# Optimization experiments

Measured on AMD Instinct MI355X. Metric: run time of the kernel, lower is better.

## Reference

```python
import jax, jax.numpy as jnp
import numpy as np

N_NODES = 50000
N_EDGES = 800000
IN_CH = 64
HID_CH = 128


def setup_inputs() -> dict:
    key = jax.random.key(0)
    k1, k2, k3 = jax.random.split(key, 3)
    x = jax.random.normal(k1, (N_NODES, IN_CH), dtype=jnp.float32)
    edge_index = jax.random.randint(k2, (2, N_EDGES), 0, N_NODES, dtype=jnp.int64)
    # lin_l weight of SAGEConv: [hidden_channels, in_channels]
    W = jax.random.normal(k3, (HID_CH, IN_CH), dtype=jnp.float32) * (1.0 / np.sqrt(IN_CH))
    return {"x": x, "edge_index": edge_index, "W": W}


def reference(x, edge_index, W):
    src = edge_index[0]  # message sources
    dst = edge_index[1]  # aggregation targets
    msgs = x[src]  # [E, in] gather
    summed = jax.ops.segment_sum(msgs, dst, num_segments=N_NODES)  # [N, in]
    counts = jax.ops.segment_sum(jnp.ones((msgs.shape[0],), dtype=x.dtype), dst,
                                 num_segments=N_NODES)  # [N]
    mean = summed / jnp.maximum(counts, 1.0)[:, None]  # mean aggregation (0 for isolated nodes)
    # lin_l: no bias, no root_weight -> out = mean @ W^T
    return jnp.einsum('ni,oi->no', mean, W)
```

## Files before the change

### kernel.cpp

```cpp
#include <hip/hip_runtime.h>


constexpr int N_NODES = 50000;
constexpr int N_EDGES = 800000;
constexpr int IN_CH   = 64;
constexpr int HID_CH  = 128;

constexpr int NBKT          = 256;
constexpr int NODES_PER_BKT = 196;
constexpr int BKT_CAP       = 4096;
constexpr int CHUNK         = 4096;
constexpr int NBIN_BLOCKS   = (N_EDGES + CHUNK - 1) / CHUNK;

__global__ __launch_bounds__(256) void bin_kernel(
    const int* __restrict__ ei,
    int* __restrict__ cursor,
    unsigned long long* __restrict__ binned)
{
    __shared__ int hist[NBKT];
    __shared__ int scan[NBKT];
    __shared__ int lexcl[NBKT];
    __shared__ int lcur[NBKT];
    __shared__ int res[NBKT];
    __shared__ unsigned long long stage[CHUNK];

    const int t  = threadIdx.x;
    const int e0 = blockIdx.x * CHUNK;
    const int nE = min(N_EDGES - e0, CHUNK);

    hist[t] = 0;
    __syncthreads();

    int srcs[16], dsts[16];
    #pragma unroll
    for (int q = 0; q < 4; ++q) {
        const int idx = t * 16 + q * 4;
        if (idx < nE) {
            const int4 s4 = *reinterpret_cast<const int4*>(ei + e0 + idx);
            const int4 d4 = *reinterpret_cast<const int4*>(ei + N_EDGES + e0 + idx);
            srcs[q * 4 + 0] = s4.x; srcs[q * 4 + 1] = s4.y;
            srcs[q * 4 + 2] = s4.z; srcs[q * 4 + 3] = s4.w;
            dsts[q * 4 + 0] = d4.x; dsts[q * 4 + 1] = d4.y;
            dsts[q * 4 + 2] = d4.z; dsts[q * 4 + 3] = d4.w;
            atomicAdd(&hist[d4.x / NODES_PER_BKT], 1);
            atomicAdd(&hist[d4.y / NODES_PER_BKT], 1);
            atomicAdd(&hist[d4.z / NODES_PER_BKT], 1);
            atomicAdd(&hist[d4.w / NODES_PER_BKT], 1);
        } else {
            srcs[q*4+0]=srcs[q*4+1]=srcs[q*4+2]=srcs[q*4+3]=0;
            dsts[q*4+0]=dsts[q*4+1]=dsts[q*4+2]=dsts[q*4+3]=0;
        }
    }
    __syncthreads();

    const int hv = hist[t];
    scan[t] = hv;
    __syncthreads();
    for (int off = 1; off < NBKT; off <<= 1) {
        const int u = (t >= off) ? scan[t - off] : 0;
        __syncthreads();
        scan[t] += u;
        __syncthreads();
    }
    const int myExcl = scan[t] - hv;
    lexcl[t] = myExcl;
    lcur[t]  = myExcl;
    res[t]   = (hv > 0) ? atomicAdd(&cursor[t], hv) : 0;
    __syncthreads();

    #pragma unroll
    for (int q = 0; q < 16; ++q) {
        const int idx = t * 16 + q;
        if (idx < nE) {
            const int bkt = dsts[q] / NODES_PER_BKT;
            const int p = atomicAdd(&lcur[bkt], 1);
            stage[p] = ((unsigned long long)(unsigned)dsts[q] << 32) | (unsigned)srcs[q];
        }
    }
    __syncthreads();

    for (int i = t; i < nE; i += 256) {
        const unsigned long long v = stage[i];
        const int bkt = (int)(v >> 32) / NODES_PER_BKT;
        const int p = res[bkt] + (i - lexcl[bkt]);
        if (p < BKT_CAP) binned[(size_t)bkt * BKT_CAP + p] = v;
    }
}

__global__ __launch_bounds__(256) void csr_build_kernel(
    const unsigned long long* __restrict__ binned,
    const int* __restrict__ cursor,
    int* __restrict__ offs,
    int* __restrict__ deg,
    int* __restrict__ csr_src)
{
    __shared__ int bsum[NBKT];
    __shared__ int ldeg[NODES_PER_BKT];
    __shared__ int lscan[NBKT];
    __shared__ int lcur[NODES_PER_BKT];
    __shared__ int stage_src[BKT_CAP];

    const int b = blockIdx.x;
    const int t = threadIdx.x;

    const int cAll = min(cursor[t], BKT_CAP);
    bsum[t] = cAll;
    if (t < NODES_PER_BKT) ldeg[t] = 0;
    __syncthreads();
    for (int off = 1; off < NBKT; off <<= 1) {
        const int u = (t >= off) ? bsum[t - off] : 0;
        __syncthreads();
        bsum[t] += u;
        __syncthreads();
    }
    const int cnt   = min(cursor[b], BKT_CAP);
    const int ebase = bsum[b] - cnt;
    const int nodeBase = b * NODES_PER_BKT;

    unsigned long long ev[16];
    #pragma unroll
    for (int q = 0; q < 16; ++q) {
        const int i = t + q * 256;
        ev[q] = 0;
        if (i < cnt) {
            ev[q] = binned[(size_t)b * BKT_CAP + i];
            atomicAdd(&ldeg[(int)(ev[q] >> 32) - nodeBase], 1);
        }
    }
    __syncthreads();

    const int dv = (t < NODES_PER_BKT) ? ldeg[t] : 0;
    lscan[t] = dv;
    __syncthreads();
    for (int off = 1; off < NBKT; off <<= 1) {
        const int u = (t >= off) ? lscan[t - off] : 0;
        __syncthreads();
        lscan[t] += u;
        __syncthreads();
    }
    const int nNodes = min(N_NODES - nodeBase, NODES_PER_BKT);
    if (t < nNodes) {
        const int excl = lscan[t] - dv;
        offs[nodeBase + t] = ebase + excl;
        deg[nodeBase + t]  = dv;
        lcur[t] = excl;
    }
    if (b == NBKT - 1 && t == 0) offs[N_NODES] = N_EDGES;
    __syncthreads();

    #pragma unroll
    for (int q = 0; q < 16; ++q) {
        const int i = t + q * 256;
        if (i < cnt) {
            const int loc = (int)(ev[q] >> 32) - nodeBase;
            const int p = atomicAdd(&lcur[loc], 1);
            stage_src[p] = (int)(ev[q] & 0xffffffffu);
        }
    }
    __syncthreads();

    for (int i = t; i < cnt; i += 256) {
        csr_src[ebase + i] = stage_src[i];
    }
}

__global__ __launch_bounds__(256) void gather_sum_kernel(
    const float* __restrict__ x,
    const int*   __restrict__ csr_src,
    const int*   __restrict__ offs,
    float*       __restrict__ sums)
{
    const int wave = threadIdx.x >> 6;
    const int lane = threadIdx.x & 63;
    const int grp  = lane >> 4;
    const int ch4  = lane & 15;
    const int wid0 = blockIdx.x * 4 + wave;
    const int nw   = gridDim.x * 4;

    for (int n = wid0; n < N_NODES; n += nw) {
        const int start = offs[n];
        const int end   = offs[n + 1];
        float a0 = 0.f, a1 = 0.f, a2 = 0.f, a3 = 0.f;

        for (int base = start; base < end; base += 64) {
            const int cnt = min(end - base, 64);
            int idx = 0;
            if (lane < cnt) idx = csr_src[base + lane];
            const int nIt = (cnt + 3) >> 2;
            for (int i = 0; i < nIt; i += 4) {
                const int e0 = 4 * i + grp;
                const int e1 = e0 + 4, e2 = e0 + 8, e3 = e0 + 12;
                const int s0 = __shfl(idx, e0 & 63, 64);
                const int s1 = __shfl(idx, e1 & 63, 64);
                const int s2 = __shfl(idx, e2 & 63, 64);
                const int s3 = __shfl(idx, e3 & 63, 64);
                const float f0 = (e0 < cnt) ? 1.f : 0.f;
                const float f1 = (e1 < cnt) ? 1.f : 0.f;
                const float f2 = (e2 < cnt) ? 1.f : 0.f;
                const float f3 = (e3 < cnt) ? 1.f : 0.f;
                const float4 v0 = *reinterpret_cast<const float4*>(x + (size_t)s0 * IN_CH + ch4 * 4);
                const float4 v1 = *reinterpret_cast<const float4*>(x + (size_t)s1 * IN_CH + ch4 * 4);
                const float4 v2 = *reinterpret_cast<const float4*>(x + (size_t)s2 * IN_CH + ch4 * 4);
                const float4 v3 = *reinterpret_cast<const float4*>(x + (size_t)s3 * IN_CH + ch4 * 4);
                a0 = fmaf(f0, v0.x, a0); a1 = fmaf(f0, v0.y, a1);
                a2 = fmaf(f0, v0.z, a2); a3 = fmaf(f0, v0.w, a3);
                a0 = fmaf(f1, v1.x, a0); a1 = fmaf(f1, v1.y, a1);
                a2 = fmaf(f1, v1.z, a2); a3 = fmaf(f1, v1.w, a3);
                a0 = fmaf(f2, v2.x, a0); a1 = fmaf(f2, v2.y, a1);
                a2 = fmaf(f2, v2.z, a2); a3 = fmaf(f2, v2.w, a3);
                a0 = fmaf(f3, v3.x, a0); a1 = fmaf(f3, v3.y, a1);
                a2 = fmaf(f3, v3.z, a2); a3 = fmaf(f3, v3.w, a3);
            }
        }
        #pragma unroll
        for (int m = 16; m <= 32; m <<= 1) {
            a0 += __shfl_xor(a0, m, 64);
            a1 += __shfl_xor(a1, m, 64);
            a2 += __shfl_xor(a2, m, 64);
            a3 += __shfl_xor(a3, m, 64);
        }
        if (lane < 16) {
            float4 r{a0, a1, a2, a3};
            *reinterpret_cast<float4*>(sums + (size_t)n * IN_CH + ch4 * 4) = r;
        }
    }
}

__global__ __launch_bounds__(256) void gemm_kernel(
    const float* __restrict__ sums,
    const int*   __restrict__ deg,
    const float* __restrict__ W,
    float*       __restrict__ out)
{
    __shared__ float4 sW4[16][HID_CH + 1];
    __shared__ float4 sA4[16][16];

    const int t = threadIdx.x;
    #pragma unroll
    for (int r = 0; r < 8; ++r) {
        int i = t + r * 256;
        int o = i >> 4, k4 = i & 15;
        sW4[k4][o] = *reinterpret_cast<const float4*>(W + (size_t)o * IN_CH + k4 * 4);
    }
    const int n0 = blockIdx.x * 16;
    {
        int node = n0 + (t >> 4);
        int k4 = t & 15;
        float4 v = *reinterpret_cast<const float4*>(sums + (size_t)node * IN_CH + k4 * 4);
        float inv = 1.0f / fmaxf((float)deg[node], 1.0f);
        v.x *= inv; v.y *= inv; v.z *= inv; v.w *= inv;
        sA4[t >> 4][k4] = v;
    }
    __syncthreads();

    const int wave = t >> 6;
    const int lane = t & 63;
    const int nb = wave * 4;

    float acc[4][2] = {{0.f, 0.f}, {0.f, 0.f}, {0.f, 0.f}, {0.f, 0.f}};
    #pragma unroll
    for (int k4 = 0; k4 < 16; ++k4) {
        const float4 w0 = sW4[k4][lane];
        const float4 w1 = sW4[k4][lane + 64];
        #pragma unroll
        for (int j = 0; j < 4; ++j) {
            const float4 a = sA4[nb + j][k4];
            acc[j][0] += a.x * w0.x + a.y * w0.y + a.z * w0.z + a.w * w0.w;
            acc[j][1] += a.x * w1.x + a.y * w1.y + a.z * w1.z + a.w * w1.w;
        }
    }
    #pragma unroll
    for (int j = 0; j < 4; ++j) {
        const size_t row = (size_t)(n0 + nb + j) * HID_CH;
        out[row + lane]      = acc[j][0];
        out[row + 64 + lane] = acc[j][1];
    }
}

extern "C" void kernel_launch(void* const* d_in, const int* in_sizes, int n_in,
                              void* d_out, int out_size, void* d_ws, size_t ws_size,
                              hipStream_t stream) {
    const float* x   = (const float*)d_in[0];
    const int*   ei  = (const int*)  d_in[1];
    const float* W   = (const float*)d_in[2];
    float*       out = (float*)d_out;

    unsigned long long* binned = (unsigned long long*)d_ws;
    int*   cursor  = (int*)(binned + (size_t)NBKT * BKT_CAP);
    int*   offs    = cursor + NBKT;
    int*   deg     = offs + 50004;
    int*   csr_src = deg + N_NODES;
    float* sums    = (float*)(csr_src + N_EDGES);

    hipMemsetAsync(cursor, 0, NBKT * sizeof(int), stream);
    bin_kernel<<<NBIN_BLOCKS, 256, 0, stream>>>(ei, cursor, binned);
    csr_build_kernel<<<NBKT, 256, 0, stream>>>(binned, cursor, offs, deg, csr_src);
    gather_sum_kernel<<<N_NODES / 16, 256, 0, stream>>>(x, csr_src, offs, sums);
    gemm_kernel<<<N_NODES / 16, 256, 0, stream>>>(sums, deg, W, out);
}
```

Measured before the change: 142.1 us.

## Fuse CSR build, gather-sum and GEMM into one per-sub-bucket kernel

Replaces the three kernels after binning with a single kernel where each block takes a quarter of a bucket's nodes. The block counts degrees and orders source indices in LDS, gathers and averages neighbour rows, and multiplies by W kept in shared memory, all without writing offsets, CSR or sums to global memory. This removes two launches and the global round trips of the intermediate buffers. In exchange, each block re-reads its whole bucket (four times redundant), reloads W, runs only 1024 blocks, and caps staged edges at 1024 per sub-bucket.

```diff
diff --git a/kernel.cpp b/kernel.cpp
--- a/kernel.cpp
+++ b/kernel.cpp
@@ -11,6 +11,10 @@
 constexpr int BKT_CAP       = 4096;
 constexpr int CHUNK         = 4096;
 constexpr int NBIN_BLOCKS   = (N_EDGES + CHUNK - 1) / CHUNK;
+
+constexpr int SUB  = 4;
+constexpr int NPS  = NODES_PER_BKT / SUB;
+constexpr int SCAP = 1024;
 
 __global__ __launch_bounds__(256) void bin_kernel(
     const int* __restrict__ ei,
@@ -87,193 +91,139 @@
     }
 }
 
-__global__ __launch_bounds__(256) void csr_build_kernel(
+__global__ __launch_bounds__(256) void fused_kernel(
     const unsigned long long* __restrict__ binned,
     const int* __restrict__ cursor,
-    int* __restrict__ offs,
-    int* __restrict__ deg,
-    int* __restrict__ csr_src)
+    const float* __restrict__ x,
+    const float* __restrict__ W,
+    float* __restrict__ out)
 {
-    __shared__ int bsum[NBKT];
-    __shared__ int ldeg[NODES_PER_BKT];
-    __shared__ int lscan[NBKT];
-    __shared__ int lcur[NODES_PER_BKT];
-    __shared__ int stage_src[BKT_CAP];
-
-    const int b = blockIdx.x;
-    const int t = threadIdx.x;
-
-    const int cAll = min(cursor[t], BKT_CAP);
-    bsum[t] = cAll;
-    if (t < NODES_PER_BKT) ldeg[t] = 0;
-    __syncthreads();
-    for (int off = 1; off < NBKT; off <<= 1) {
-        const int u = (t >= off) ? bsum[t - off] : 0;
-        __syncthreads();
-        bsum[t] += u;
-        __syncthreads();
-    }
-    const int cnt   = min(cursor[b], BKT_CAP);
-    const int ebase = bsum[b] - cnt;
-    const int nodeBase = b * NODES_PER_BKT;
+    __shared__ float4 sW4[16][HID_CH + 1];
+    __shared__ int   ldeg[64];
+    __shared__ int   loffs[64];
+    __shared__ int   lcur[64];
+    __shared__ int   stage_src[SCAP];
+    __shared__ float4 sA4[4][4][16];
+
+    const int bb  = blockIdx.x;
+    const int b   = bb >> 2;
+    const int sub = bb & 3;
+    const int lo  = b * NODES_PER_BKT + sub * NPS;
+    const int t   = threadIdx.x;
+
+    #pragma unroll
+    for (int r = 0; r < 8; ++r) {
+        const int i = t + r * 256;
+        const int o = i >> 4, k4 = i & 15;
+        sW4[k4][o] = *reinterpret_cast<const float4*>(W + (size_t)o * IN_CH + k4 * 4);
+    }
+    if (t < 64) ldeg[t] = 0;
+    __syncthreads();
+
+    const int cnt = min(cursor[b], BKT_CAP);
 
     unsigned long long ev[16];
     #pragma unroll
     for (int q = 0; q < 16; ++q) {
         const int i = t + q * 256;
-        ev[q] = 0;
-        if (i < cnt) {
-            ev[q] = binned[(size_t)b * BKT_CAP + i];
-            atomicAdd(&ldeg[(int)(ev[q] >> 32) - nodeBase], 1);
-        }
-    }
-    __syncthreads();
-
-    const int dv = (t < NODES_PER_BKT) ? ldeg[t] : 0;
-    lscan[t] = dv;
-    __syncthreads();
-    for (int off = 1; off < NBKT; off <<= 1) {
-        const int u = (t >= off) ? lscan[t - off] : 0;
-        __syncthreads();
-        lscan[t] += u;
-        __syncthreads();
-    }
-    const int nNodes = min(N_NODES - nodeBase, NODES_PER_BKT);
-    if (t < nNodes) {
-        const int excl = lscan[t] - dv;
-        offs[nodeBase + t] = ebase + excl;
-        deg[nodeBase + t]  = dv;
-        lcur[t] = excl;
-    }
-    if (b == NBKT - 1 && t == 0) offs[N_NODES] = N_EDGES;
-    __syncthreads();
-
-    #pragma unroll
-    for (int q = 0; q < 16; ++q) {
-        const int i = t + q * 256;
-        if (i < cnt) {
-            const int loc = (int)(ev[q] >> 32) - nodeBase;
+        ev[q] = 0xffffffff00000000ull;
+        if (i < cnt) ev[q] = binned[(size_t)b * BKT_CAP + i];
+    }
+    #pragma unroll
+    for (int q = 0; q < 16; ++q) {
+        const int loc = (int)(ev[q] >> 32) - lo;
+        if ((unsigned)loc < (unsigned)NPS) atomicAdd(&ldeg[loc], 1);
+    }
+    __syncthreads();
+
+    if (t < 64) {
+        const int v = ldeg[t];
+        int incl = v;
+        #pragma unroll
+        for (int off = 1; off < 64; off <<= 1) {
+            const int u = __shfl_up(incl, off, 64);
+            incl += (t >= off) ? u : 0;
+        }
+        loffs[t] = incl - v;
+        lcur[t]  = incl - v;
+    }
+    __syncthreads();
+
+    #pragma unroll
+    for (int q = 0; q < 16; ++q) {
+        const int loc = (int)(ev[q] >> 32) - lo;
+        if ((unsigned)loc < (unsigned)NPS) {
             const int p = atomicAdd(&lcur[loc], 1);
-            stage_src[p] = (int)(ev[q] & 0xffffffffu);
-        }
-    }
-    __syncthreads();
-
-    for (int i = t; i < cnt; i += 256) {
-        csr_src[ebase + i] = stage_src[i];
-    }
-}
-
-__global__ __launch_bounds__(256) void gather_sum_kernel(
-    const float* __restrict__ x,
-    const int*   __restrict__ csr_src,
-    const int*   __restrict__ offs,
-    float*       __restrict__ sums)
-{
-    const int wave = threadIdx.x >> 6;
-    const int lane = threadIdx.x & 63;
+            if (p < SCAP) stage_src[p] = (int)(ev[q] & 0xffffffffu);
+        }
+    }
+    __syncthreads();
+
+    const int wave = t >> 6;
+    const int lane = t & 63;
     const int grp  = lane >> 4;
     const int ch4  = lane & 15;
-    const int wid0 = blockIdx.x * 4 + wave;
-    const int nw   = gridDim.x * 4;
-
-    for (int n = wid0; n < N_NODES; n += nw) {
-        const int start = offs[n];
-        const int end   = offs[n + 1];
-        float a0 = 0.f, a1 = 0.f, a2 = 0.f, a3 = 0.f;
-
-        for (int base = start; base < end; base += 64) {
-            const int cnt = min(end - base, 64);
-            int idx = 0;
-            if (lane < cnt) idx = csr_src[base + lane];
-            const int nIt = (cnt + 3) >> 2;
-            for (int i = 0; i < nIt; i += 4) {
-                const int e0 = 4 * i + grp;
-                const int e1 = e0 + 4, e2 = e0 + 8, e3 = e0 + 12;
-                const int s0 = __shfl(idx, e0 & 63, 64);
-                const int s1 = __shfl(idx, e1 & 63, 64);
-                const int s2 = __shfl(idx, e2 & 63, 64);
-                const int s3 = __shfl(idx, e3 & 63, 64);
-                const float f0 = (e0 < cnt) ? 1.f : 0.f;
-                const float f1 = (e1 < cnt) ? 1.f : 0.f;
-                const float f2 = (e2 < cnt) ? 1.f : 0.f;
-                const float f3 = (e3 < cnt) ? 1.f : 0.f;
-                const float4 v0 = *reinterpret_cast<const float4*>(x + (size_t)s0 * IN_CH + ch4 * 4);
-                const float4 v1 = *reinterpret_cast<const float4*>(x + (size_t)s1 * IN_CH + ch4 * 4);
-                const float4 v2 = *reinterpret_cast<const float4*>(x + (size_t)s2 * IN_CH + ch4 * 4);
-                const float4 v3 = *reinterpret_cast<const float4*>(x + (size_t)s3 * IN_CH + ch4 * 4);
-                a0 = fmaf(f0, v0.x, a0); a1 = fmaf(f0, v0.y, a1);
-                a2 = fmaf(f0, v0.z, a2); a3 = fmaf(f0, v0.w, a3);
-                a0 = fmaf(f1, v1.x, a0); a1 = fmaf(f1, v1.y, a1);
-                a2 = fmaf(f1, v1.z, a2); a3 = fmaf(f1, v1.w, a3);
-                a0 = fmaf(f2, v2.x, a0); a1 = fmaf(f2, v2.y, a1);
-                a2 = fmaf(f2, v2.z, a2); a3 = fmaf(f2, v2.w, a3);
-                a0 = fmaf(f3, v3.x, a0); a1 = fmaf(f3, v3.y, a1);
-                a2 = fmaf(f3, v3.z, a2); a3 = fmaf(f3, v3.w, a3);
-            }
-        }
-        #pragma unroll
-        for (int m = 16; m <= 32; m <<= 1) {
-            a0 += __shfl_xor(a0, m, 64);
-            a1 += __shfl_xor(a1, m, 64);
-            a2 += __shfl_xor(a2, m, 64);
-            a3 += __shfl_xor(a3, m, 64);
-        }
-        if (lane < 16) {
-            float4 r{a0, a1, a2, a3};
-            *reinterpret_cast<float4*>(sums + (size_t)n * IN_CH + ch4 * 4) = r;
-        }
-    }
-}
-
-__global__ __launch_bounds__(256) void gemm_kernel(
-    const float* __restrict__ sums,
-    const int*   __restrict__ deg,
-    const float* __restrict__ W,
-    float*       __restrict__ out)
-{
-    __shared__ float4 sW4[16][HID_CH + 1];
-    __shared__ float4 sA4[16][16];
-
-    const int t = threadIdx.x;
-    #pragma unroll
-    for (int r = 0; r < 8; ++r) {
-        int i = t + r * 256;
-        int o = i >> 4, k4 = i & 15;
-        sW4[k4][o] = *reinterpret_cast<const float4*>(W + (size_t)o * IN_CH + k4 * 4);
-    }
-    const int n0 = blockIdx.x * 16;
-    {
-        int node = n0 + (t >> 4);
-        int k4 = t & 15;
-        float4 v = *reinterpret_cast<const float4*>(sums + (size_t)node * IN_CH + k4 * 4);
-        float inv = 1.0f / fmaxf((float)deg[node], 1.0f);
-        v.x *= inv; v.y *= inv; v.z *= inv; v.w *= inv;
-        sA4[t >> 4][k4] = v;
-    }
-    __syncthreads();
-
-    const int wave = t >> 6;
-    const int lane = t & 63;
-    const int nb = wave * 4;
-
-    float acc[4][2] = {{0.f, 0.f}, {0.f, 0.f}, {0.f, 0.f}, {0.f, 0.f}};
-    #pragma unroll
-    for (int k4 = 0; k4 < 16; ++k4) {
-        const float4 w0 = sW4[k4][lane];
-        const float4 w1 = sW4[k4][lane + 64];
+
+    for (int nb = 0; nb < 64; nb += 16) {
         #pragma unroll
         for (int j = 0; j < 4; ++j) {
-            const float4 a = sA4[nb + j][k4];
-            acc[j][0] += a.x * w0.x + a.y * w0.y + a.z * w0.z + a.w * w0.w;
-            acc[j][1] += a.x * w1.x + a.y * w1.y + a.z * w1.z + a.w * w1.w;
-        }
-    }
-    #pragma unroll
-    for (int j = 0; j < 4; ++j) {
-        const size_t row = (size_t)(n0 + nb + j) * HID_CH;
-        out[row + lane]      = acc[j][0];
-        out[row + 64 + lane] = acc[j][1];
+            const int loc = nb + j * 4 + wave;
+            float a0 = 0.f, a1 = 0.f, a2 = 0.f, a3 = 0.f;
+            int d = 0;
+            if (loc < NPS) d = ldeg[loc];
+            const int beg = (loc < NPS) ? loffs[loc] : 0;
+            for (int i = 0; i < d; i += 8) {
+                const int eA = i + grp;
+                const int eB = i + 4 + grp;
+                const int sA = stage_src[beg + min(eA, d - 1)];
+                const int sB = stage_src[beg + min(eB, d - 1)];
+                const float fA = (eA < d) ? 1.f : 0.f;
+                const float fB = (eB < d) ? 1.f : 0.f;
+                const float4 vA = *reinterpret_cast<const float4*>(x + (size_t)sA * IN_CH + ch4 * 4);
+                const float4 vB = *reinterpret_cast<const float4*>(x + (size_t)sB * IN_CH + ch4 * 4);
+                a0 = fmaf(fA, vA.x, a0); a1 = fmaf(fA, vA.y, a1);
+                a2 = fmaf(fA, vA.z, a2); a3 = fmaf(fA, vA.w, a3);
+                a0 = fmaf(fB, vB.x, a0); a1 = fmaf(fB, vB.y, a1);
+                a2 = fmaf(fB, vB.z, a2); a3 = fmaf(fB, vB.w, a3);
+            }
+            #pragma unroll
+            for (int m = 16; m <= 32; m <<= 1) {
+                a0 += __shfl_xor(a0, m, 64);
+                a1 += __shfl_xor(a1, m, 64);
+                a2 += __shfl_xor(a2, m, 64);
+                a3 += __shfl_xor(a3, m, 64);
+            }
+            if (lane < 16) {
+                const float inv = 1.0f / fmaxf((float)d, 1.0f);
+                float4 r{a0 * inv, a1 * inv, a2 * inv, a3 * inv};
+                sA4[wave][j][ch4] = r;
+            }
+        }
+        __asm__ volatile("s_waitcnt lgkmcnt(0)" ::: "memory");
+        __builtin_amdgcn_sched_barrier(0);
+
+        float acc[4][2] = {{0.f,0.f},{0.f,0.f},{0.f,0.f},{0.f,0.f}};
+        #pragma unroll
+        for (int k4 = 0; k4 < 16; ++k4) {
+            const float4 w0 = sW4[k4][lane];
+            const float4 w1 = sW4[k4][lane + 64];
+            #pragma unroll
+            for (int j = 0; j < 4; ++j) {
+                const float4 a = sA4[wave][j][k4];
+                acc[j][0] += a.x * w0.x + a.y * w0.y + a.z * w0.z + a.w * w0.w;
+                acc[j][1] += a.x * w1.x + a.y * w1.y + a.z * w1.z + a.w * w1.w;
+            }
+        }
+        #pragma unroll
+        for (int j = 0; j < 4; ++j) {
+            const int loc = nb + j * 4 + wave;
+            const int n = lo + loc;
+            if (loc < NPS && n < N_NODES) {
+                const size_t row = (size_t)n * HID_CH;
+                out[row + lane]      = acc[j][0];
+                out[row + 64 + lane] = acc[j][1];
+            }
+        }
     }
 }
 
@@ -286,15 +236,9 @@
     float*       out = (float*)d_out;
 
     unsigned long long* binned = (unsigned long long*)d_ws;
-    int*   cursor  = (int*)(binned + (size_t)NBKT * BKT_CAP);
-    int*   offs    = cursor + NBKT;
-    int*   deg     = offs + 50004;
-    int*   csr_src = deg + N_NODES;
-    float* sums    = (float*)(csr_src + N_EDGES);
+    int* cursor = (int*)(binned + (size_t)NBKT * BKT_CAP);
 
     hipMemsetAsync(cursor, 0, NBKT * sizeof(int), stream);
     bin_kernel<<<NBIN_BLOCKS, 256, 0, stream>>>(ei, cursor, binned);
-    csr_build_kernel<<<NBKT, 256, 0, stream>>>(binned, cursor, offs, deg, csr_src);
-    gather_sum_kernel<<<N_NODES / 16, 256, 0, stream>>>(x, csr_src, offs, sums);
-    gemm_kernel<<<N_NODES / 16, 256, 0, stream>>>(sums, deg, W, out);
+    fused_kernel<<<NBKT * SUB, 256, 0, stream>>>(binned, cursor, x, W, out);
 }
```

New measurement: 190.5 us. +34.1%, slower.

## Fuse neighbor gather-sum with mean normalization and linear projection

Applied to the files above, without the earlier changes.

Merges the gather-sum and GEMM kernels into one. Each wave aggregates a node, divides by the degree taken from the CSR offsets, stages the mean row in LDS, and multiplies it by W held in shared memory. This drops the intermediate sums buffer, the deg array and one kernel launch. In exchange every block loads all of W into LDS, which costs extra LDS traffic per block and may lower occupancy. Each wave now handles a fixed set of four nodes instead of a grid-stride loop.

```diff
diff --git a/kernel.cpp b/kernel.cpp
--- a/kernel.cpp
+++ b/kernel.cpp
@@ -10,7 +10,7 @@
 constexpr int NODES_PER_BKT = 196;
 constexpr int BKT_CAP       = 4096;
 constexpr int CHUNK         = 4096;
-constexpr int NBIN_BLOCKS   = (N_EDGES + CHUNK - 1) / CHUNK;
+constexpr int NBIN          = (N_EDGES + CHUNK - 1) / CHUNK;
 
 __global__ __launch_bounds__(256) void bin_kernel(
     const int* __restrict__ ei,
@@ -72,8 +72,8 @@
     for (int q = 0; q < 16; ++q) {
         const int idx = t * 16 + q;
         if (idx < nE) {
-            const int bkt = dsts[q] / NODES_PER_BKT;
-            const int p = atomicAdd(&lcur[bkt], 1);
+            const int b = dsts[q] / NODES_PER_BKT;
+            const int p = atomicAdd(&lcur[b], 1);
             stage[p] = ((unsigned long long)(unsigned)dsts[q] << 32) | (unsigned)srcs[q];
         }
     }
@@ -81,9 +81,9 @@
 
     for (int i = t; i < nE; i += 256) {
         const unsigned long long v = stage[i];
-        const int bkt = (int)(v >> 32) / NODES_PER_BKT;
-        const int p = res[bkt] + (i - lexcl[bkt]);
-        if (p < BKT_CAP) binned[(size_t)bkt * BKT_CAP + p] = v;
+        const int b = (int)(v >> 32) / NODES_PER_BKT;
+        const int p = res[b] + (i - lexcl[b]);
+        if (p < BKT_CAP) binned[(size_t)b * BKT_CAP + p] = v;
     }
 }
 
@@ -91,7 +91,6 @@
     const unsigned long long* __restrict__ binned,
     const int* __restrict__ cursor,
     int* __restrict__ offs,
-    int* __restrict__ deg,
     int* __restrict__ csr_src)
 {
     __shared__ int bsum[NBKT];
@@ -142,7 +141,6 @@
     if (t < nNodes) {
         const int excl = lscan[t] - dv;
         offs[nodeBase + t] = ebase + excl;
-        deg[nodeBase + t]  = dv;
         lcur[t] = excl;
     }
     if (b == NBKT - 1 && t == 0) offs[N_NODES] = N_EDGES;
@@ -164,24 +162,39 @@
     }
 }
 
-__global__ __launch_bounds__(256) void gather_sum_kernel(
+__global__ __launch_bounds__(256) void gather_fused_kernel(
     const float* __restrict__ x,
     const int*   __restrict__ csr_src,
     const int*   __restrict__ offs,
-    float*       __restrict__ sums)
+    const float* __restrict__ W,
+    float*       __restrict__ out)
 {
-    const int wave = threadIdx.x >> 6;
-    const int lane = threadIdx.x & 63;
+    __shared__ float4 sW4[16][HID_CH + 1];
+    __shared__ float4 sM[4][16];
+
+    const int t = threadIdx.x;
+    #pragma unroll
+    for (int r = 0; r < 8; ++r) {
+        const int i = t + r * 256;
+        const int o = i >> 4, k4 = i & 15;
+        sW4[k4][o] = *reinterpret_cast<const float4*>(W + (size_t)o * IN_CH + k4 * 4);
+    }
+    __syncthreads();
+
+    const int wave = t >> 6;
+    const int lane = t & 63;
     const int grp  = lane >> 4;
     const int ch4  = lane & 15;
-    const int wid0 = blockIdx.x * 4 + wave;
-    const int nw   = gridDim.x * 4;
-
-    for (int n = wid0; n < N_NODES; n += nw) {
+    const int wid  = blockIdx.x * 4 + wave;
+
+    #pragma unroll 1
+    for (int j = 0; j < 4; ++j) {
+        const int n = wid * 4 + j;
         const int start = offs[n];
         const int end   = offs[n + 1];
+        const int d     = end - start;
+
         float a0 = 0.f, a1 = 0.f, a2 = 0.f, a3 = 0.f;
-
         for (int base = start; base < end; base += 64) {
             const int cnt = min(end - base, 64);
             int idx = 0;
@@ -219,61 +232,26 @@
             a2 += __shfl_xor(a2, m, 64);
             a3 += __shfl_xor(a3, m, 64);
         }
+        const float inv = 1.0f / fmaxf((float)d, 1.0f);
         if (lane < 16) {
-            float4 r{a0, a1, a2, a3};
-            *reinterpret_cast<float4*>(sums + (size_t)n * IN_CH + ch4 * 4) = r;
-        }
-    }
-}
-
-__global__ __launch_bounds__(256) void gemm_kernel(
-    const float* __restrict__ sums,
-    const int*   __restrict__ deg,
-    const float* __restrict__ W,
-    float*       __restrict__ out)
-{
-    __shared__ float4 sW4[16][HID_CH + 1];
-    __shared__ float4 sA4[16][16];
-
-    const int t = threadIdx.x;
-    #pragma unroll
-    for (int r = 0; r < 8; ++r) {
-        int i = t + r * 256;
-        int o = i >> 4, k4 = i & 15;
-        sW4[k4][o] = *reinterpret_cast<const float4*>(W + (size_t)o * IN_CH + k4 * 4);
-    }
-    const int n0 = blockIdx.x * 16;
-    {
-        int node = n0 + (t >> 4);
-        int k4 = t & 15;
-        float4 v = *reinterpret_cast<const float4*>(sums + (size_t)node * IN_CH + k4 * 4);
-        float inv = 1.0f / fmaxf((float)deg[node], 1.0f);
-        v.x *= inv; v.y *= inv; v.z *= inv; v.w *= inv;
-        sA4[t >> 4][k4] = v;
-    }
-    __syncthreads();
-
-    const int wave = t >> 6;
-    const int lane = t & 63;
-    const int nb = wave * 4;
-
-    float acc[4][2] = {{0.f, 0.f}, {0.f, 0.f}, {0.f, 0.f}, {0.f, 0.f}};
-    #pragma unroll
-    for (int k4 = 0; k4 < 16; ++k4) {
-        const float4 w0 = sW4[k4][lane];
-        const float4 w1 = sW4[k4][lane + 64];
+            float4 r{a0 * inv, a1 * inv, a2 * inv, a3 * inv};
+            sM[wave][ch4] = r;
+        }
+        __asm__ volatile("s_waitcnt lgkmcnt(0)" ::: "memory");
+        __builtin_amdgcn_sched_barrier(0);
+
+        float o0 = 0.f, o1 = 0.f;
         #pragma unroll
-        for (int j = 0; j < 4; ++j) {
-            const float4 a = sA4[nb + j][k4];
-            acc[j][0] += a.x * w0.x + a.y * w0.y + a.z * w0.z + a.w * w0.w;
-            acc[j][1] += a.x * w1.x + a.y * w1.y + a.z * w1.z + a.w * w1.w;
-        }
-    }
-    #pragma unroll
-    for (int j = 0; j < 4; ++j) {
-        const size_t row = (size_t)(n0 + nb + j) * HID_CH;
-        out[row + lane]      = acc[j][0];
-        out[row + 64 + lane] = acc[j][1];
+        for (int k4 = 0; k4 < 16; ++k4) {
+            const float4 w0 = sW4[k4][lane];
+            const float4 w1 = sW4[k4][lane + 64];
+            const float4 a  = sM[wave][k4];
+            o0 += a.x * w0.x + a.y * w0.y + a.z * w0.z + a.w * w0.w;
+            o1 += a.x * w1.x + a.y * w1.y + a.z * w1.z + a.w * w1.w;
+        }
+        const size_t row = (size_t)n * HID_CH;
+        out[row + lane]      = o0;
+        out[row + 64 + lane] = o1;
     }
 }
 
@@ -286,15 +264,12 @@
     float*       out = (float*)d_out;
 
     unsigned long long* binned = (unsigned long long*)d_ws;
-    int*   cursor  = (int*)(binned + (size_t)NBKT * BKT_CAP);
-    int*   offs    = cursor + NBKT;
-    int*   deg     = offs + 50004;
-    int*   csr_src = deg + N_NODES;
-    float* sums    = (float*)(csr_src + N_EDGES);
+    int* cursor  = (int*)(binned + (size_t)NBKT * BKT_CAP);
+    int* offs    = cursor + NBKT;
+    int* csr_src = offs + 50004;
 
     hipMemsetAsync(cursor, 0, NBKT * sizeof(int), stream);
-    bin_kernel<<<NBIN_BLOCKS, 256, 0, stream>>>(ei, cursor, binned);
-    csr_build_kernel<<<NBKT, 256, 0, stream>>>(binned, cursor, offs, deg, csr_src);
-    gather_sum_kernel<<<N_NODES / 16, 256, 0, stream>>>(x, csr_src, offs, sums);
-    gemm_kernel<<<N_NODES / 16, 256, 0, stream>>>(sums, deg, W, out);
-}
+    bin_kernel<<<NBIN, 256, 0, stream>>>(ei, cursor, binned);
+    csr_build_kernel<<<NBKT, 256, 0, stream>>>(binned, cursor, offs, csr_src);
+    gather_fused_kernel<<<N_NODES / 16, 256, 0, stream>>>(x, csr_src, offs, W, out);
+}
```

Result: no change. 141.8 us (-0.2%).
